# Kernel tuning notes

Measured on AMD Instinct MI355X. Metric: run time of the kernel, lower is better.

Reference implementation:

```python
import jax, jax.numpy as jnp
import numpy as np


def _mlp2(x, w1, b1, w2, b2):
    # 2-layer MLP with exact GELU (matches torch nn.GELU default)
    h = jax.nn.gelu(x @ w1 + b1, approximate=False)
    return h @ w2 + b2


def setup_inputs() -> dict:
    B, nx = 16, 16384
    d_latent, d_hidden, k = 64, 128, 3
    key = jax.random.key(0)
    ks = jax.random.split(key, 14)
    s = 0.1
    inp = {
        "u0": jax.random.normal(ks[0], (B, nx), dtype=jnp.float32),
        "x": jax.random.uniform(ks[1], (B, nx), dtype=jnp.float32),
        # node_mlp: 2 -> d_hidden -> d_latent
        "node_w1": jax.random.normal(ks[2], (2, d_hidden), dtype=jnp.float32) * s,
        "node_b1": jnp.zeros((d_hidden,), dtype=jnp.float32),
        "node_w2": jax.random.normal(ks[3], (d_hidden, d_latent), dtype=jnp.float32) * s,
        "node_b2": jnp.zeros((d_latent,), dtype=jnp.float32),
        # edge_mlp: 3 -> d_hidden -> d_latent
        "edge_w1": jax.random.normal(ks[4], (3, d_hidden), dtype=jnp.float32) * s,
        "edge_b1": jnp.zeros((d_hidden,), dtype=jnp.float32),
        "edge_w2": jax.random.normal(ks[5], (d_hidden, d_latent), dtype=jnp.float32) * s,
        "edge_b2": jnp.zeros((d_latent,), dtype=jnp.float32),
        # combine: 2*d_latent -> d_hidden -> d_latent
        "comb_w1": jax.random.normal(ks[6], (2 * d_latent, d_hidden), dtype=jnp.float32) * s,
        "comb_b1": jnp.zeros((d_hidden,), dtype=jnp.float32),
        "comb_w2": jax.random.normal(ks[7], (d_hidden, d_latent), dtype=jnp.float32) * s,
        "comb_b2": jnp.zeros((d_latent,), dtype=jnp.float32),
        "k": k,
    }
    return inp


def reference(u0, x, node_w1, node_b1, node_w2, node_b2,
              edge_w1, edge_b1, edge_w2, edge_b2,
              comb_w1, comb_b1, comb_w2, comb_b2, k):
    B, nx = u0.shape
    # h_self = node_mlp([u_i, x_i])                       -> [B, nx, d_latent]
    h_self = _mlp2(jnp.stack([u0, x], axis=-1), node_w1, node_b1, node_w2, node_b2)

    # Replicate-padded neighbor gather == clamp indices to [0, nx-1]
    offs = jnp.arange(-k, k + 1)                          # [2k+1]
    idx = jnp.clip(jnp.arange(nx)[None, :] + offs[:, None], 0, nx - 1)  # [2k+1, nx]
    u_j = u0[:, idx]                                      # [B, 2k+1, nx]
    dx = x[:, idx] - x[:, None, :]                        # [B, 2k+1, nx]
    u_i = jnp.broadcast_to(u0[:, None, :], u_j.shape)

    # edge_mlp over all neighbors at once, then sum over neighbor axis
    edge_in = jnp.stack([u_i, u_j, dx], axis=-1)          # [B, 2k+1, nx, 3]
    agg = _mlp2(edge_in, edge_w1, edge_b1, edge_w2, edge_b2).sum(axis=1)  # [B, nx, d_latent]

    return _mlp2(jnp.concatenate([h_self, agg], axis=-1), comb_w1, comb_b1, comb_w2, comb_b2)
```

## Files before the change

### kernel.cpp

```cpp
#include <hip/hip_runtime.h>
#include <hip/hip_bf16.h>

#define NXc 16384
#define DHc 128
#define DLc 64
#define Kc  3
#define Wc  7
#define Pc  32
#define NTc 256
#define HALO 38
#define RB  272

typedef __attribute__((ext_vector_type(8))) short short8;
typedef __attribute__((ext_vector_type(4))) float f32x4;
typedef __attribute__((ext_vector_type(2))) float f32x2;

#define OFF_U  0
#define OFF_X  160
#define OFF_GN 320
#define OFF_H2 OFF_GN
#define OFF_S  9024
#define OFF_HC 17728
#define SMEM_BYTES 26432

#define WS_NW2 0
#define WS_EW2 8192
#define WS_CW1 16384
#define WS_CW2 32768
#define WS_TOTAL 40960

#if __has_builtin(__builtin_amdgcn_exp2f)
#define EXP2F(x) __builtin_amdgcn_exp2f(x)
#else
#define EXP2F(x) exp2f(x)
#endif
#if __has_builtin(__builtin_amdgcn_rcpf)
#define RCPF(x) __builtin_amdgcn_rcpf(x)
#else
#define RCPF(x) (1.0f / (x))
#endif

#define GC0 -2.30220838f
#define GC1 -0.10294325f

__device__ __forceinline__ f32x2 vfma(f32x2 a, f32x2 b, f32x2 c) {
    return __builtin_elementwise_fma(a, b, c);
}
__device__ __forceinline__ f32x2 splat2(float s) { f32x2 v = {s, s}; return v; }

__device__ __forceinline__ f32x2 gelu2v(f32x2 xv) {
    xv = __builtin_elementwise_max(xv, splat2(-8.0f));
    f32x2 z = xv * vfma(splat2(GC1), xv * xv, splat2(GC0));
    f32x2 t;
    t.x = EXP2F(z.x);
    t.y = EXP2F(z.y);
    t = t + splat2(1.0f);
    float rr = RCPF(t.x * t.y);
    f32x2 ts = {t.y, t.x};
    return xv * ts * splat2(rr);
}

__device__ __forceinline__ void gelu2_accv(f32x2 xv, f32x2& acc) {
    f32x2 z = xv * vfma(splat2(GC1), xv * xv, splat2(GC0));
    f32x2 t;
    t.x = EXP2F(z.x);
    t.y = EXP2F(z.y);
    t = t + splat2(1.0f);
    float rr = RCPF(t.x * t.y);
    f32x2 ts = {t.y, t.x};
    acc = vfma(xv * ts, splat2(rr), acc);
}

#if __has_builtin(__builtin_amdgcn_cvt_pk_bf16_f32)
typedef __attribute__((ext_vector_type(2))) __bf16 bf16x2_t;
__device__ __forceinline__ unsigned pack_bf16(float a, float b) {
    bf16x2_t v = __builtin_amdgcn_cvt_pk_bf16_f32(a, b);
    unsigned r; __builtin_memcpy(&r, &v, 4); return r;
}
#else
__device__ __forceinline__ unsigned bf16rne(float a) {
    unsigned u;
    __builtin_memcpy(&u, &a, 4);
    return u + 0x7FFFu + ((u >> 16) & 1u);
}
__device__ __forceinline__ unsigned pack_bf16(float a, float b) {
    return (bf16rne(a) >> 16) | (bf16rne(b) & 0xFFFF0000u);
}
#endif
__device__ __forceinline__ void store_bf16x4(void* p, float a, float b, float c, float d) {
    uint2 u;
    u.x = pack_bf16(a, b);
    u.y = pack_bf16(c, d);
    *(uint2*)p = u;
}

__global__ void pack_weights(const float* __restrict__ nw2, const float* __restrict__ ew2,
                             const float* __restrict__ cw1, const float* __restrict__ cw2,
                             __hip_bfloat16* __restrict__ ws)
{
    int idx = blockIdx.x * 256 + threadIdx.x;
    const float* src;
    int N, base, e;
    if (idx < 8192)       { src = nw2; N = 64;  base = WS_NW2; e = idx; }
    else if (idx < 16384) { src = ew2; N = 64;  base = WS_EW2; e = idx - 8192; }
    else if (idx < 32768) { src = cw1; N = 128; base = WS_CW1; e = idx - 16384; }
    else                  { src = cw2; N = 64;  base = WS_CW2; e = idx - 32768; }
    int f = e >> 9, l = (e >> 3) & 63, j = e & 7;
    int nt = f >> 2, kt = f & 3;
    int k = kt * 32 + (l >> 4) * 8 + j;
    int n = nt * 16 + (l & 15);
    ws[base + e] = __float2bfloat16(src[k * N + n]);
}

__global__ __launch_bounds__(NTc, 6)
void lifting_mfma(const float* __restrict__ u0, const float* __restrict__ x,
                  const float* __restrict__ nw1, const float* __restrict__ nb1,
                  const float* __restrict__ nb2, const float* __restrict__ eb1,
                  const float* __restrict__ eb2, const float* __restrict__ cb1,
                  const float* __restrict__ cb2, const float* __restrict__ ew1,
                  const short8* __restrict__ wsv, float* __restrict__ out)
{
    __shared__ char sm[SMEM_BYTES];
    float* s_u = (float*)(sm + OFF_U);
    float* s_x = (float*)(sm + OFF_X);

    const int tid   = threadIdx.x;
    const int wave  = tid >> 6;
    const int lane  = tid & 63;
    const int quad  = lane >> 4;
    const int l15   = lane & 15;
    const int tiles = NXc / Pc;
    const int b     = blockIdx.x / tiles;
    const int i0    = (blockIdx.x % tiles) * Pc;
    const float* ub = u0 + (size_t)b * NXc;
    const float* xb = x  + (size_t)b * NXc;

    if (tid < HALO) {
        int i = i0 - Kc + tid;
        i = i < 0 ? 0 : (i >= NXc ? NXc - 1 : i);
        s_u[tid] = ub[i];
        s_x[tid] = xb[i];
    }
    __syncthreads();

    {
        const int jq = tid & 31;
        const int pbase = (tid >> 5) * 4;
        const int j0 = jq * 4;
        const f32x2 w0l = *(const f32x2*)(nw1 + j0),           w0h = *(const f32x2*)(nw1 + j0 + 2);
        const f32x2 w1l = *(const f32x2*)(nw1 + DHc + j0),     w1h = *(const f32x2*)(nw1 + DHc + j0 + 2);
        const f32x2 nbl = *(const f32x2*)(nb1 + j0),           nbh = *(const f32x2*)(nb1 + j0 + 2);
        const f32x2 e0l = *(const f32x2*)(ew1 + j0),           e0h = *(const f32x2*)(ew1 + j0 + 2);
        const f32x2 e1l = *(const f32x2*)(ew1 + DHc + j0),     e1h = *(const f32x2*)(ew1 + DHc + j0 + 2);
        const f32x2 e2l = *(const f32x2*)(ew1 + 2 * DHc + j0), e2h = *(const f32x2*)(ew1 + 2 * DHc + j0 + 2);
        const f32x2 bel = *(const f32x2*)(eb1 + j0),           beh = *(const f32x2*)(eb1 + j0 + 2);

        float su[10], sx[10];
        #pragma unroll
        for (int r = 0; r < 10; ++r) {
            su[r] = s_u[pbase + r];
            sx[r] = s_x[pbase + r];
        }

        f32x2 cwl[10], cwh[10];
        #pragma unroll
        for (int r = 0; r < 10; ++r) {
            f32x2 uv = splat2(su[r]), xv = splat2(sx[r]);
            cwl[r] = vfma(uv, e1l, xv * e2l);
            cwh[r] = vfma(uv, e1h, xv * e2h);
        }

        #pragma unroll
        for (int r0 = 0; r0 < 4; ++r0) {
            const int p = pbase + r0;
            const f32x2 uv = splat2(su[r0 + 3]), xv = splat2(sx[r0 + 3]);

            f32x2 gl = gelu2v(vfma(uv, w0l, vfma(xv, w1l, nbl)));
            f32x2 gh = gelu2v(vfma(uv, w0h, vfma(xv, w1h, nbh)));
            store_bf16x4(sm + OFF_GN + p * RB + j0 * 2, gl.x, gl.y, gh.x, gh.y);

            f32x2 al = vfma(uv, e0l, bel - xv * e2l);
            f32x2 ah = vfma(uv, e0h, beh - xv * e2h);
            f32x2 accl = {0.f, 0.f}, acch = {0.f, 0.f};
            #pragma unroll
            for (int o = 0; o < Wc; ++o) {
                gelu2_accv(al + cwl[r0 + o], accl);
                gelu2_accv(ah + cwh[r0 + o], acch);
            }
            store_bf16x4(sm + OFF_S + p * RB + j0 * 2, accl.x, accl.y, acch.x, acch.y);
        }
    }
    __syncthreads();

    {
        const int mt = wave & 1, mat = wave >> 1;
        const int rowbase = mt * 16;
        const int aoff = mat ? OFF_S : OFF_GN;
        const short8* Bmat = wsv + (mat ? (WS_EW2 >> 3) : (WS_NW2 >> 3));
        f32x4 acc[4] = {{0,0,0,0},{0,0,0,0},{0,0,0,0},{0,0,0,0}};
        #pragma unroll
        for (int kt = 0; kt < 4; ++kt) {
            short8 af = *(const short8*)(sm + aoff + (rowbase + l15) * RB + kt * 64 + quad * 16);
            #pragma unroll
            for (int nt = 0; nt < 4; ++nt) {
                short8 wf = Bmat[(nt * 4 + kt) * 64 + lane];
                acc[nt] = __builtin_amdgcn_mfma_f32_16x16x32_bf16(wf, af, acc[nt], 0, 0, 0);
            }
        }
        const float* bias = mat ? eb2 : nb2;
        const float bscale = mat ? 7.f : 1.f;
        const int colhalf = mat ? DLc : 0;
        const int p = rowbase + l15;
        #pragma unroll
        for (int nt = 0; nt < 4; ++nt) {
            float4 bv = ((const float4*)bias)[nt * 4 + quad];
            store_bf16x4(sm + OFF_HC + p * RB + (colhalf + nt * 16 + quad * 4) * 2,
                         fmaf(bscale, bv.x, acc[nt][0]),
                         fmaf(bscale, bv.y, acc[nt][1]),
                         fmaf(bscale, bv.z, acc[nt][2]),
                         fmaf(bscale, bv.w, acc[nt][3]));
        }
    }
    __syncthreads();

    {
        const int mt = wave & 1, nh = wave >> 1;
        const int rowbase = mt * 16;
        const short8* Bmat = wsv + (WS_CW1 >> 3);
        f32x4 acc[4] = {{0,0,0,0},{0,0,0,0},{0,0,0,0},{0,0,0,0}};
        #pragma unroll
        for (int kt = 0; kt < 4; ++kt) {
            short8 af = *(const short8*)(sm + OFF_HC + (rowbase + l15) * RB + kt * 64 + quad * 16);
            #pragma unroll
            for (int t = 0; t < 4; ++t) {
                int nt = nh * 4 + t;
                short8 wf = Bmat[(nt * 4 + kt) * 64 + lane];
                acc[t] = __builtin_amdgcn_mfma_f32_16x16x32_bf16(wf, af, acc[t], 0, 0, 0);
            }
        }
        const int p = rowbase + l15;
        #pragma unroll
        for (int t = 0; t < 4; ++t) {
            int nbase = (nh * 4 + t) * 16 + quad * 4;
            float4 cb = ((const float4*)cb1)[nbase >> 2];
            f32x2 pl = {acc[t][0] + cb.x, acc[t][1] + cb.y};
            f32x2 ph = {acc[t][2] + cb.z, acc[t][3] + cb.w};
            f32x2 hl = gelu2v(pl), hh = gelu2v(ph);
            store_bf16x4(sm + OFF_H2 + p * RB + nbase * 2, hl.x, hl.y, hh.x, hh.y);
        }
    }
    __syncthreads();

    {
        const int mt = wave & 1, nh = wave >> 1;
        const int rowbase = mt * 16;
        const short8* Bmat = wsv + (WS_CW2 >> 3);
        f32x4 acc[2] = {{0,0,0,0},{0,0,0,0}};
        #pragma unroll
        for (int kt = 0; kt < 4; ++kt) {
            short8 af = *(const short8*)(sm + OFF_H2 + (rowbase + l15) * RB + kt * 64 + quad * 16);
            #pragma unroll
            for (int t = 0; t < 2; ++t) {
                int nt = nh * 2 + t;
                short8 wf = Bmat[(nt * 4 + kt) * 64 + lane];
                acc[t] = __builtin_amdgcn_mfma_f32_16x16x32_bf16(wf, af, acc[t], 0, 0, 0);
            }
        }
        const int p = rowbase + l15;
        float* outb = out + ((size_t)b * NXc + i0 + p) * DLc;
        #pragma unroll
        for (int t = 0; t < 2; ++t) {
            int nbase = (nh * 2 + t) * 16 + quad * 4;
            float4 cb = ((const float4*)cb2)[nbase >> 2];
            float4 v;
            v.x = acc[t][0] + cb.x;
            v.y = acc[t][1] + cb.y;
            v.z = acc[t][2] + cb.z;
            v.w = acc[t][3] + cb.w;
            *(float4*)(outb + nbase) = v;
        }
    }
}

extern "C" void kernel_launch(void* const* d_in, const int* in_sizes, int n_in,
                              void* d_out, int out_size, void* d_ws, size_t ws_size,
                              hipStream_t stream) {
    const float* u0  = (const float*)d_in[0];
    const float* x   = (const float*)d_in[1];
    const float* nw1 = (const float*)d_in[2];
    const float* nb1 = (const float*)d_in[3];
    const float* nw2 = (const float*)d_in[4];
    const float* nb2 = (const float*)d_in[5];
    const float* ew1 = (const float*)d_in[6];
    const float* eb1 = (const float*)d_in[7];
    const float* ew2 = (const float*)d_in[8];
    const float* eb2 = (const float*)d_in[9];
    const float* cw1 = (const float*)d_in[10];
    const float* cb1 = (const float*)d_in[11];
    const float* cw2 = (const float*)d_in[12];
    const float* cb2 = (const float*)d_in[13];
    float* out = (float*)d_out;

    __hip_bfloat16* ws = (__hip_bfloat16*)d_ws;
    pack_weights<<<WS_TOTAL / 256, 256, 0, stream>>>(nw2, ew2, cw1, cw2, ws);

    const int grid = 16 * (NXc / Pc);
    lifting_mfma<<<grid, NTc, 0, stream>>>(u0, x, nw1, nb1, nb2, eb1, eb2, cb1, cb2,
                                           ew1, (const short8*)d_ws, out);
}
```

Baseline: 200.8 us.

## Fold node/edge output layers into combine first layer via precomputed weight products

Precomputes nw2·cw1_top and ew2·cw1_bottom (plus folded biases) in a small setup kernel, so the main kernel goes straight from the hidden GELU activations to the combine hidden layer. This removes one MFMA stage, one LDS round trip and one barrier per tile. The fused stage now does two MFMAs per output tile over 128-wide K, so MFMA count stays similar but bf16 rounding of the intermediate latent is gone. The fold kernel runs serial 64-term dot products in 9 blocks, which adds some setup latency.

```diff
diff --git a/kernel.cpp b/kernel.cpp
--- a/kernel.cpp
+++ b/kernel.cpp
@@ -18,16 +18,14 @@
 #define OFF_U  0
 #define OFF_X  160
 #define OFF_GN 320
-#define OFF_H2 OFF_GN
 #define OFF_S  9024
-#define OFF_HC 17728
+#define OFF_H2 17728
 #define SMEM_BYTES 26432
 
-#define WS_NW2 0
-#define WS_EW2 8192
-#define WS_CW1 16384
+#define WS_M1  0
+#define WS_M2  16384
 #define WS_CW2 32768
-#define WS_TOTAL 40960
+#define FB_OFF_BYTES  81920
 
 #if __has_builtin(__builtin_amdgcn_exp2f)
 #define EXP2F(x) __builtin_amdgcn_exp2f(x)
@@ -94,31 +92,64 @@
     *(uint2*)p = u;
 }
 
-__global__ void pack_weights(const float* __restrict__ nw2, const float* __restrict__ ew2,
-                             const float* __restrict__ cw1, const float* __restrict__ cw2,
-                             __hip_bfloat16* __restrict__ ws)
+__global__ void fold_pack(const float* __restrict__ nw2, const float* __restrict__ ew2,
+                          const float* __restrict__ cw1, const float* __restrict__ cw2,
+                          const float* __restrict__ nb2, const float* __restrict__ eb2,
+                          const float* __restrict__ cb1, __hip_bfloat16* __restrict__ ws,
+                          float* __restrict__ fb)
 {
-    int idx = blockIdx.x * 256 + threadIdx.x;
-    const float* src;
-    int N, base, e;
-    if (idx < 8192)       { src = nw2; N = 64;  base = WS_NW2; e = idx; }
-    else if (idx < 16384) { src = ew2; N = 64;  base = WS_EW2; e = idx - 8192; }
-    else if (idx < 32768) { src = cw1; N = 128; base = WS_CW1; e = idx - 16384; }
-    else                  { src = cw2; N = 64;  base = WS_CW2; e = idx - 32768; }
-    int f = e >> 9, l = (e >> 3) & 63, j = e & 7;
-    int nt = f >> 2, kt = f & 3;
-    int k = kt * 32 + (l >> 4) * 8 + j;
-    int n = nt * 16 + (l & 15);
-    ws[base + e] = __float2bfloat16(src[k * N + n]);
+    __shared__ float slab[32][DHc];
+    const int tid = threadIdx.x;
+    const int blk = blockIdx.x;
+
+    if (blk < 8) {
+        const int mat = blk >> 2, kt = blk & 3;
+        const float* head  = mat ? ew2 : nw2;
+        const float* crows = mat ? (cw1 + 64 * DHc) : cw1;
+        for (int idx = tid; idx < 32 * DHc; idx += NTc) {
+            int kl = idx >> 7, n = idx & 127;
+            int k = kt * 32 + kl;
+            float acc = 0.f;
+            for (int q = 0; q < 64; ++q)
+                acc = fmaf(head[k * 64 + q], crows[q * DHc + n], acc);
+            slab[kl][n] = acc;
+        }
+        __syncthreads();
+        const int matbase = mat ? WS_M2 : WS_M1;
+        for (int idx = tid; idx < 8 * 512; idx += NTc) {
+            int nt = idx >> 9, r = idx & 511;
+            int l = r >> 3, j = r & 7;
+            int kl = (l >> 4) * 8 + j;
+            int n = nt * 16 + (l & 15);
+            ws[matbase + (nt * 4 + kt) * 512 + r] = __float2bfloat16(slab[kl][n]);
+        }
+    } else {
+        for (int e = tid; e < 8192; e += NTc) {
+            int f = e >> 9, l = (e >> 3) & 63, j = e & 7;
+            int nt = f >> 2, kt = f & 3;
+            int k = kt * 32 + (l >> 4) * 8 + j;
+            int n = nt * 16 + (l & 15);
+            ws[WS_CW2 + e] = __float2bfloat16(cw2[k * DLc + n]);
+        }
+        if (tid < DHc) {
+            int n = tid;
+            float acc = cb1[n];
+            for (int q = 0; q < 64; ++q)
+                acc = fmaf(nb2[q], cw1[q * DHc + n], acc);
+            for (int q = 0; q < 64; ++q)
+                acc = fmaf(7.0f * eb2[q], cw1[(64 + q) * DHc + n], acc);
+            fb[n] = acc;
+        }
+    }
 }
 
 __global__ __launch_bounds__(NTc, 6)
 void lifting_mfma(const float* __restrict__ u0, const float* __restrict__ x,
                   const float* __restrict__ nw1, const float* __restrict__ nb1,
-                  const float* __restrict__ nb2, const float* __restrict__ eb1,
-                  const float* __restrict__ eb2, const float* __restrict__ cb1,
-                  const float* __restrict__ cb2, const float* __restrict__ ew1,
-                  const short8* __restrict__ wsv, float* __restrict__ out)
+                  const float* __restrict__ eb1, const float* __restrict__ ew1,
+                  const float* __restrict__ cb2,
+                  const short8* __restrict__ wsv, const float* __restrict__ fbp,
+                  float* __restrict__ out)
 {
     __shared__ char sm[SMEM_BYTES];
     float* s_u = (float*)(sm + OFF_U);
@@ -193,56 +224,29 @@
     __syncthreads();
 
     {
-        const int mt = wave & 1, mat = wave >> 1;
-        const int rowbase = mt * 16;
-        const int aoff = mat ? OFF_S : OFF_GN;
-        const short8* Bmat = wsv + (mat ? (WS_EW2 >> 3) : (WS_NW2 >> 3));
-        f32x4 acc[4] = {{0,0,0,0},{0,0,0,0},{0,0,0,0},{0,0,0,0}};
-        #pragma unroll
-        for (int kt = 0; kt < 4; ++kt) {
-            short8 af = *(const short8*)(sm + aoff + (rowbase + l15) * RB + kt * 64 + quad * 16);
-            #pragma unroll
-            for (int nt = 0; nt < 4; ++nt) {
-                short8 wf = Bmat[(nt * 4 + kt) * 64 + lane];
-                acc[nt] = __builtin_amdgcn_mfma_f32_16x16x32_bf16(wf, af, acc[nt], 0, 0, 0);
-            }
-        }
-        const float* bias = mat ? eb2 : nb2;
-        const float bscale = mat ? 7.f : 1.f;
-        const int colhalf = mat ? DLc : 0;
-        const int p = rowbase + l15;
-        #pragma unroll
-        for (int nt = 0; nt < 4; ++nt) {
-            float4 bv = ((const float4*)bias)[nt * 4 + quad];
-            store_bf16x4(sm + OFF_HC + p * RB + (colhalf + nt * 16 + quad * 4) * 2,
-                         fmaf(bscale, bv.x, acc[nt][0]),
-                         fmaf(bscale, bv.y, acc[nt][1]),
-                         fmaf(bscale, bv.z, acc[nt][2]),
-                         fmaf(bscale, bv.w, acc[nt][3]));
-        }
-    }
-    __syncthreads();
-
-    {
         const int mt = wave & 1, nh = wave >> 1;
         const int rowbase = mt * 16;
-        const short8* Bmat = wsv + (WS_CW1 >> 3);
+        const short8* M1 = wsv + (WS_M1 >> 3);
+        const short8* M2 = wsv + (WS_M2 >> 3);
         f32x4 acc[4] = {{0,0,0,0},{0,0,0,0},{0,0,0,0},{0,0,0,0}};
         #pragma unroll
         for (int kt = 0; kt < 4; ++kt) {
-            short8 af = *(const short8*)(sm + OFF_HC + (rowbase + l15) * RB + kt * 64 + quad * 16);
+            short8 ag = *(const short8*)(sm + OFF_GN + (rowbase + l15) * RB + kt * 64 + quad * 16);
+            short8 as = *(const short8*)(sm + OFF_S  + (rowbase + l15) * RB + kt * 64 + quad * 16);
             #pragma unroll
             for (int t = 0; t < 4; ++t) {
                 int nt = nh * 4 + t;
-                short8 wf = Bmat[(nt * 4 + kt) * 64 + lane];
-                acc[t] = __builtin_amdgcn_mfma_f32_16x16x32_bf16(wf, af, acc[t], 0, 0, 0);
+                short8 m1f = M1[(nt * 4 + kt) * 64 + lane];
+                short8 m2f = M2[(nt * 4 + kt) * 64 + lane];
+                acc[t] = __builtin_amdgcn_mfma_f32_16x16x32_bf16(m1f, ag, acc[t], 0, 0, 0);
+                acc[t] = __builtin_amdgcn_mfma_f32_16x16x32_bf16(m2f, as, acc[t], 0, 0, 0);
             }
         }
         const int p = rowbase + l15;
         #pragma unroll
         for (int t = 0; t < 4; ++t) {
             int nbase = (nh * 4 + t) * 16 + quad * 4;
-            float4 cb = ((const float4*)cb1)[nbase >> 2];
+            float4 cb = ((const float4*)fbp)[nbase >> 2];
             f32x2 pl = {acc[t][0] + cb.x, acc[t][1] + cb.y};
             f32x2 ph = {acc[t][2] + cb.z, acc[t][3] + cb.w};
             f32x2 hl = gelu2v(pl), hh = gelu2v(ph);
@@ -302,9 +306,11 @@
     float* out = (float*)d_out;
 
     __hip_bfloat16* ws = (__hip_bfloat16*)d_ws;
-    pack_weights<<<WS_TOTAL / 256, 256, 0, stream>>>(nw2, ew2, cw1, cw2, ws);
+    float* fb = (float*)((char*)d_ws + FB_OFF_BYTES);
+
+    fold_pack<<<9, NTc, 0, stream>>>(nw2, ew2, cw1, cw2, nb2, eb2, cb1, ws, fb);
 
     const int grid = 16 * (NXc / Pc);
-    lifting_mfma<<<grid, NTc, 0, stream>>>(u0, x, nw1, nb1, nb2, eb1, eb2, cb1, cb2,
-                                           ew1, (const short8*)d_ws, out);
-}
+    lifting_mfma<<<grid, NTc, 0, stream>>>(u0, x, nw1, nb1, eb1, ew1, cb2,
+                                           (const short8*)d_ws, fb, out);
+}
```

Result: slower. 215.0 us (+7.0%).
